# Performance work log

Measured on AMD Instinct MI355X. Metric: run time of the kernel, lower is better.

Reference implementation:

```python
import jax, jax.numpy as jnp
import numpy as np

EMBED = 1024
HEADS = 16
HEAD_DIM = EMBED // HEADS


def setup_inputs() -> dict:
    key = jax.random.key(0)
    ks = jax.random.split(key, 8)
    N, S = 4, 2048
    inp = {
        "values": jax.random.normal(ks[0], (N, S, EMBED), dtype=jnp.float32),
        "keys": jax.random.normal(ks[1], (N, S, EMBED), dtype=jnp.float32),
        "queries": jax.random.normal(ks[2], (N, S, EMBED), dtype=jnp.float32),
        # Linear weights stored as [in, out] (torch Linear applies x @ W.T; here W already transposed)
        "W_v": jax.random.normal(ks[3], (EMBED, EMBED), dtype=jnp.float32) / np.sqrt(EMBED),
        "W_k": jax.random.normal(ks[4], (EMBED, EMBED), dtype=jnp.float32) / np.sqrt(EMBED),
        "W_q": jax.random.normal(ks[5], (EMBED, EMBED), dtype=jnp.float32) / np.sqrt(EMBED),
        "W_o": jax.random.normal(ks[6], (EMBED, EMBED), dtype=jnp.float32) / np.sqrt(EMBED),
        "b_o": jax.random.normal(ks[7], (EMBED,), dtype=jnp.float32) * 0.01,
    }
    return inp


def reference(values, keys, queries, W_v, W_k, W_q, W_o, b_o):
    N, q_len, _ = queries.shape
    v = (values @ W_v).reshape(N, -1, HEADS, HEAD_DIM)   # [n, v_len, h, d]
    k = (keys @ W_k).reshape(N, -1, HEADS, HEAD_DIM)     # [n, k_len, h, d]
    q = (queries @ W_q).reshape(N, -1, HEADS, HEAD_DIM)  # [n, q_len, h, d]
    # NOTE: original scales by sqrt(embed_size), not sqrt(head_dim)
    energy = jnp.einsum('nqhd,nkhd->nhqk', q, k) / jnp.sqrt(jnp.float32(EMBED))
    attn = jax.nn.softmax(energy, axis=-1)
    out = jnp.einsum('nhqk,nkhd->nqhd', attn, v).reshape(N, q_len, EMBED)
    return out @ W_o + b_o
```

## Files before the change

kernel.cpp:

```cpp
#include <hip/hip_runtime.h>
#include <hip/hip_bf16.h>
#include <stdint.h>

typedef __attribute__((ext_vector_type(8))) short short8;
typedef __attribute__((ext_vector_type(4))) float f32x4;
typedef __attribute__((ext_vector_type(4))) unsigned short u16x4;
typedef unsigned short u16;

#define EMBED 1024
#define SEQ 2048
#define NBATCH 4
#define MROWS (NBATCH * SEQ)

__device__ __forceinline__ u16 f2bf(float f) {
  union { float f; uint32_t u; } v; v.f = f;
  uint32_t r = v.u + 0x7fffu + ((v.u >> 16) & 1u);
  return (u16)(r >> 16);
}

__device__ __forceinline__ uint32_t cvtpk(float lo, float hi) {
  uint32_t r;
  asm("v_cvt_pk_bf16_f32 %0, %1, %2" : "=v"(r) : "v"(lo), "v"(hi));
  return r;
}

__device__ __forceinline__ float vexp2(float x) {
  float r;
  asm("v_exp_f32 %0, %1" : "=v"(r) : "v"(x));
  return r;
}

__device__ __forceinline__ void gld16(const void* g, void* l) {
  __builtin_amdgcn_global_load_lds((const __attribute__((address_space(1))) void*)g,
                                   (__attribute__((address_space(3))) void*)l, 16, 0, 0);
}

__global__ __launch_bounds__(256) void prep_kernel(const float* __restrict__ W0,
                                                   const float* __restrict__ W1,
                                                   const float* __restrict__ W2,
                                                   const float* __restrict__ W3,
                                                   u16* __restrict__ T0,
                                                   u16* __restrict__ T1,
                                                   u16* __restrict__ T2,
                                                   u16* __restrict__ T3) {
  int id = blockIdx.x;
  int z = id >> 10;
  const float* W = z == 0 ? W0 : (z == 1 ? W1 : (z == 2 ? W2 : W3));
  u16* Wt = z == 0 ? T0 : (z == 1 ? T1 : (z == 2 ? T2 : T3));
  __shared__ float tile[32][33];
  int bx = (id & 31) * 32, by = ((id >> 5) & 31) * 32;
  int tx = threadIdx.x & 31, ty = threadIdx.x >> 5;
#pragma unroll
  for (int i = 0; i < 32; i += 8)
    tile[ty + i][tx] = W[(size_t)(by + ty + i) * EMBED + bx + tx];
  __syncthreads();
#pragma unroll
  for (int i = 0; i < 32; i += 8)
    Wt[(size_t)(bx + ty + i) * EMBED + by + tx] = f2bf(tile[tx][ty + i]);
}

__global__ __launch_bounds__(256) void qkv_gemm(const float* __restrict__ Aq,
                                                const float* __restrict__ Ak,
                                                const float* __restrict__ Av,
                                                const u16* __restrict__ Wqt,
                                                const u16* __restrict__ Wkt,
                                                const u16* __restrict__ Wvt,
                                                u16* __restrict__ Qb,
                                                u16* __restrict__ Kb,
                                                u16* __restrict__ Vtb,
                                                float qscale) {
  constexpr int K = 1024;
  __shared__ float lsAf[128 * 64];
  __shared__ u16 lsB[128 * 64];

  const int id = blockIdx.x;
  const int xcd = id & 7;
  const int rest = id >> 3;
  const int bx = rest & 7;
  const int p = (rest >> 3) * 8 + xcd;
  const int z = p >> 6;
  const int by = p & 63;

  const float* A = z == 0 ? Aq : (z == 1 ? Ak : Av);
  const u16* Bt  = z == 0 ? Wqt : (z == 1 ? Wkt : Wvt);
  u16* outp      = z == 0 ? Qb : (z == 1 ? Kb : Vtb);
  const float oscale = z == 0 ? qscale : 1.0f;
  const int epi = (z == 2) ? 1 : 0;

  const int t = threadIdx.x, l = t & 63, w = t >> 6;
  const int g = l >> 4, r15 = l & 15;
  const int m0 = by * 128, n0 = bx * 128;
  const int wm = (w >> 1) * 64, wn = (w & 1) * 64;
  f32x4 acc[4][4] = {};

  const int srow = t >> 3;
  const int sc16 = (t & 7) * 16;
  const u16* Bp[4];
#pragma unroll
  for (int j = 0; j < 4; ++j) {
    int row = srow + j * 32;
    int colswz = (sc16 ^ ((row & 7) << 4)) >> 1;
    Bp[j] = Bt + (size_t)(n0 + row) * K + colswz;
  }

  const int arow_b = t >> 4;
  const int au = t & 15;
  const float* Apf[8];
#pragma unroll
  for (int j = 0; j < 8; ++j) {
    int row = j * 16 + arow_b;
    int s = ((row & 7) << 1) | ((row >> 3) & 1);
    Apf[j] = A + (size_t)(m0 + row) * K + (au ^ s) * 4;
  }

  for (int k0 = 0; k0 < K; k0 += 64) {
#pragma unroll
    for (int j = 0; j < 4; ++j)
      gld16(Bp[j] + k0, lsB + j * 2048 + w * 512);
#pragma unroll
    for (int j = 0; j < 8; ++j)
      gld16(Apf[j] + k0, (char*)lsAf + j * 4096 + w * 1024);
    __syncthreads();

    short8 af[2][4], bfv[2][4];
#pragma unroll
    for (int kk = 0; kk < 2; ++kk) {
#pragma unroll
      for (int mi = 0; mi < 4; ++mi) {
        int row = wm + mi * 16 + r15;
        int s = ((row & 7) << 1) | ((row >> 3) & 1);
        int v = kk * 8 + g * 2;
        const char* base = (const char*)lsAf + row * 256;
        f32x4 a0 = *(const f32x4*)(base + ((v ^ s) * 16));
        f32x4 a1 = *(const f32x4*)(base + (((v + 1) ^ s) * 16));
        union { uint32_t u[4]; short8 sv; } pu;
        pu.u[0] = cvtpk(a0[0], a0[1]);
        pu.u[1] = cvtpk(a0[2], a0[3]);
        pu.u[2] = cvtpk(a1[0], a1[1]);
        pu.u[3] = cvtpk(a1[2], a1[3]);
        af[kk][mi] = pu.sv;
      }
#pragma unroll
      for (int ni = 0; ni < 4; ++ni) {
        int row = wn + ni * 16 + r15;
        bfv[kk][ni] = *(const short8*)((const char*)lsB + row * 128 + ((kk * 64 + g * 16) ^ ((row & 7) << 4)));
      }
    }
#pragma unroll
    for (int kk = 0; kk < 2; ++kk)
#pragma unroll
      for (int mi = 0; mi < 4; ++mi)
#pragma unroll
        for (int ni = 0; ni < 4; ++ni)
          acc[mi][ni] = __builtin_amdgcn_mfma_f32_16x16x32_bf16(af[kk][mi], bfv[kk][ni], acc[mi][ni], 0, 0, 0);
    __syncthreads();
  }

#pragma unroll
  for (int mi = 0; mi < 4; ++mi)
#pragma unroll
    for (int ni = 0; ni < 4; ++ni)
#pragma unroll
      for (int r = 0; r < 4; ++r) {
        int row = m0 + wm + mi * 16 + g * 4 + r;
        int col = n0 + wn + ni * 16 + r15;
        float v = acc[mi][ni][r];
        if (epi == 0) {
          ((u16*)outp)[(((size_t)(row >> 11) * 16 + (col >> 6)) * SEQ + (row & 2047)) * 64 + (col & 63)] = f2bf(v * oscale);
        } else {
          ((u16*)outp)[(((size_t)(row >> 11) * 16 + (col >> 6)) * 64 + (col & 63)) * SEQ + (row & 2047)] = f2bf(v);
        }
      }
}

__global__ __launch_bounds__(256) void gemm_o(const u16* __restrict__ A,
                                              const u16* __restrict__ Bt,
                                              float* __restrict__ outp,
                                              const float* __restrict__ bias) {
  constexpr int K = 1024;
  __shared__ u16 lsA[128 * 64];
  __shared__ u16 lsB[128 * 64];

  const int id = blockIdx.x;
  const int xcd = id & 7;
  const int rest = id >> 3;
  const int bx = rest & 7;
  const int by = (rest >> 3) * 8 + xcd;

  const int t = threadIdx.x, l = t & 63, w = t >> 6;
  const int g = l >> 4, r15 = l & 15;
  const int m0 = by * 128, n0 = bx * 128;
  const int wm = (w >> 1) * 64, wn = (w & 1) * 64;
  f32x4 acc[4][4] = {};
  const int srow = t >> 3;
  const int sc16 = (t & 7) * 16;

  const u16* Ap[4]; const u16* Bp[4];
#pragma unroll
  for (int j = 0; j < 4; ++j) {
    int row = srow + j * 32;
    int colswz = (sc16 ^ ((row & 7) << 4)) >> 1;
    Ap[j] = A  + (size_t)(m0 + row) * K + colswz;
    Bp[j] = Bt + (size_t)(n0 + row) * K + colswz;
  }

  for (int k0 = 0; k0 < K; k0 += 64) {
#pragma unroll
    for (int j = 0; j < 4; ++j) {
      gld16(Ap[j] + k0, lsA + j * 2048 + w * 512);
      gld16(Bp[j] + k0, lsB + j * 2048 + w * 512);
    }
    __syncthreads();
    short8 af[2][4], bfv[2][4];
#pragma unroll
    for (int kk = 0; kk < 2; ++kk) {
#pragma unroll
      for (int mi = 0; mi < 4; ++mi) {
        int row = wm + mi * 16 + r15;
        af[kk][mi] = *(const short8*)((const char*)lsA + row * 128 + ((kk * 64 + g * 16) ^ ((row & 7) << 4)));
      }
#pragma unroll
      for (int ni = 0; ni < 4; ++ni) {
        int row = wn + ni * 16 + r15;
        bfv[kk][ni] = *(const short8*)((const char*)lsB + row * 128 + ((kk * 64 + g * 16) ^ ((row & 7) << 4)));
      }
    }
#pragma unroll
    for (int kk = 0; kk < 2; ++kk)
#pragma unroll
      for (int mi = 0; mi < 4; ++mi)
#pragma unroll
        for (int ni = 0; ni < 4; ++ni)
          acc[mi][ni] = __builtin_amdgcn_mfma_f32_16x16x32_bf16(af[kk][mi], bfv[kk][ni], acc[mi][ni], 0, 0, 0);
    __syncthreads();
  }

#pragma unroll
  for (int mi = 0; mi < 4; ++mi)
#pragma unroll
    for (int ni = 0; ni < 4; ++ni)
#pragma unroll
      for (int r = 0; r < 4; ++r) {
        int row = m0 + wm + mi * 16 + g * 4 + r;
        int col = n0 + wn + ni * 16 + r15;
        outp[(size_t)row * EMBED + col] = acc[mi][ni][r] + bias[col];
      }
}

__global__ __launch_bounds__(256) void attn_kernel(const u16* __restrict__ Q,
                                                   const u16* __restrict__ Kb,
                                                   const u16* __restrict__ Vt,
                                                   u16* __restrict__ AO) {
  __shared__ u16 lsK[2][64 * 64];
  __shared__ u16 lsV[2][64 * 64];
  const int t = threadIdx.x, l = t & 63, w = t >> 6;
  const int g = l >> 4, r15 = l & 15;

  const int flat = blockIdx.x;
  const int work = (flat & 7) * 128 + (flat >> 3);
  const int bh = work >> 4;
  const int q0 = (work & 15) * 128;

  const u16* Qh = Q + (size_t)bh * SEQ * 64;
  const u16* Kh = Kb + (size_t)bh * SEQ * 64;
  const u16* Vh = Vt + (size_t)bh * 64 * SEQ;

  short8 qf[2][2];
#pragma unroll
  for (int qi = 0; qi < 2; ++qi)
#pragma unroll
    for (int dh = 0; dh < 2; ++dh)
      qf[qi][dh] = *(const short8*)&Qh[(size_t)(q0 + w * 32 + qi * 16 + r15) * 64 + dh * 32 + g * 8];

  const short8 kones = { 0x3F80, 0x3F80, 0x3F80, 0x3F80, 0x3F80, 0x3F80, 0x3F80, 0x3F80 };
  f32x4 ssum[2] = {};
  f32x4 oacc[4][2] = {};

  const int srow = t >> 3;
  const int scolb = (t & 7) * 16;

  uint4 vreg[2];

  auto STAGE_K = [&](int buf, int kv0) {
#pragma unroll
    for (int j = 0; j < 2; ++j) {
      int row = j * 32 + srow;
      int colswz = (scolb ^ ((row & 7) << 4)) >> 1;
      gld16(Kh + (size_t)(kv0 + row) * 64 + colswz, &lsK[buf][j * 2048 + w * 512]);
    }
  };
  auto VLOAD = [&](int kv0) {
#pragma unroll
    for (int j = 0; j < 2; ++j) {
      int row = j * 32 + srow;
      vreg[j] = *(const uint4*)(Vh + (size_t)row * SEQ + kv0 + (scolb >> 1));
    }
  };
  auto VSTORE = [&](int buf) {
#pragma unroll
    for (int j = 0; j < 2; ++j) {
      int row = j * 32 + srow;
      int c4 = (row & 7) << 4, c3 = ((row >> 3) & 1) << 3;
      char* base = (char*)&lsV[buf][0] + row * 128 + (scolb ^ c4);
      *(uint2*)(base + c3)       = make_uint2(vreg[j].x, vreg[j].y);
      *(uint2*)(base + (8 ^ c3)) = make_uint2(vreg[j].z, vreg[j].w);
    }
  };

  auto STEP = [&](int buf, bool pre, int a) {
    if (pre) {
      VLOAD((a + 1) * 64);
      STAGE_K(buf ^ 1, (a + 1) * 64);
    }
    const u16* Kc = lsK[buf];
    const u16* Vc = lsV[buf];

    f32x4 sacc[2][4] = {};
    __builtin_amdgcn_s_setprio(1);
#pragma unroll
    for (int c = 0; c < 4; ++c) {
      int krow = c * 16 + r15;
      int sz = (krow & 7) << 4;
#pragma unroll
      for (int dh = 0; dh < 2; ++dh) {
        short8 kf = *(const short8*)((const char*)Kc + krow * 128 + ((dh * 64 + g * 16) ^ sz));
#pragma unroll
        for (int qi = 0; qi < 2; ++qi)
          sacc[qi][c] = __builtin_amdgcn_mfma_f32_16x16x32_bf16(kf, qf[qi][dh], sacc[qi][c], 0, 0, 0);
      }
    }
    __builtin_amdgcn_s_setprio(0);

    short8 pb[2][2];
#pragma unroll
    for (int qi = 0; qi < 2; ++qi) {
#pragma unroll
      for (int c = 0; c < 4; ++c)
#pragma unroll
        for (int r = 0; r < 4; ++r)
          sacc[qi][c][r] = vexp2(sacc[qi][c][r]);
#pragma unroll
      for (int kh = 0; kh < 2; ++kh) {
        union { uint32_t u[4]; short8 s; } pu;
        pu.u[0] = cvtpk(sacc[qi][2 * kh][0],     sacc[qi][2 * kh][1]);
        pu.u[1] = cvtpk(sacc[qi][2 * kh][2],     sacc[qi][2 * kh][3]);
        pu.u[2] = cvtpk(sacc[qi][2 * kh + 1][0], sacc[qi][2 * kh + 1][1]);
        pu.u[3] = cvtpk(sacc[qi][2 * kh + 1][2], sacc[qi][2 * kh + 1][3]);
        pb[qi][kh] = pu.s;
      }
    }
#pragma unroll
    for (int qi = 0; qi < 2; ++qi)
#pragma unroll
      for (int kh = 0; kh < 2; ++kh)
        ssum[qi] = __builtin_amdgcn_mfma_f32_16x16x32_bf16(kones, pb[qi][kh], ssum[qi], 0, 0, 0);

    __builtin_amdgcn_s_setprio(1);
#pragma unroll
    for (int dc = 0; dc < 4; ++dc) {
      int vrow = dc * 16 + r15;
      int sz = ((vrow & 7) << 4) | (((vrow >> 3) & 1) << 3);
      const char* vb = (const char*)Vc + vrow * 128;
#pragma unroll
      for (int kh = 0; kh < 2; ++kh) {
        union { uint2 v[2]; short8 s; } va;
        va.v[0] = *(const uint2*)(vb + ((kh * 64 + 8 * g) ^ sz));
        va.v[1] = *(const uint2*)(vb + ((kh * 64 + 32 + 8 * g) ^ sz));
#pragma unroll
        for (int qi = 0; qi < 2; ++qi)
          oacc[dc][qi] = __builtin_amdgcn_mfma_f32_16x16x32_bf16(va.s, pb[qi][kh], oacc[dc][qi], 0, 0, 0);
      }
    }
    __builtin_amdgcn_s_setprio(0);

    if (pre) VSTORE(buf ^ 1);
    __syncthreads();
  };

  VLOAD(0);
  STAGE_K(0, 0);
  VSTORE(0);
  __syncthreads();

#pragma unroll 1
  for (int pair = 0; pair < 16; ++pair) {
    STEP(0, true, 2 * pair);
    STEP(1, pair != 15, 2 * pair + 1);
  }

  const int nb = bh >> 4, h = bh & 15;
  float inv[2] = { 1.0f / ssum[0][0], 1.0f / ssum[1][0] };
#pragma unroll
  for (int dc = 0; dc < 4; ++dc)
#pragma unroll
    for (int qi = 0; qi < 2; ++qi) {
      int q = q0 + w * 32 + qi * 16 + r15;
      int d = dc * 16 + g * 4;
      uint32_t a = cvtpk(oacc[dc][qi][0] * inv[qi], oacc[dc][qi][1] * inv[qi]);
      uint32_t b = cvtpk(oacc[dc][qi][2] * inv[qi], oacc[dc][qi][3] * inv[qi]);
      uint2* dst = (uint2*)&AO[((size_t)(nb * SEQ + q)) * EMBED + h * 64 + d];
      *dst = make_uint2(a, b);
    }
}

extern "C" void kernel_launch(void* const* d_in, const int* in_sizes, int n_in,
                              void* d_out, int out_size, void* d_ws, size_t ws_size,
                              hipStream_t stream) {
  const float* values  = (const float*)d_in[0];
  const float* keys    = (const float*)d_in[1];
  const float* queries = (const float*)d_in[2];
  const float* W_v = (const float*)d_in[3];
  const float* W_k = (const float*)d_in[4];
  const float* W_q = (const float*)d_in[5];
  const float* W_o = (const float*)d_in[6];
  const float* b_o = (const float*)d_in[7];

  const size_t XSZ = (size_t)MROWS * EMBED;
  const size_t WSZ = (size_t)EMBED * EMBED;
  u16* ws = (u16*)d_ws;
  u16* Wvt = ws;
  u16* Wkt = Wvt + WSZ;
  u16* Wqt = Wkt + WSZ;
  u16* Wot = Wqt + WSZ;
  u16* Qb  = Wot + WSZ;
  u16* Kb  = Qb + XSZ;
  u16* Vtb = Kb + XSZ;
  u16* AO  = Vtb + XSZ;

  prep_kernel<<<4096, 256, 0, stream>>>(W_v, W_k, W_q, W_o, Wvt, Wkt, Wqt, Wot);

  const float QSCALE = 0.03125f * 1.4426950408889634f;
  qkv_gemm<<<1536, 256, 0, stream>>>(queries, keys, values, Wqt, Wkt, Wvt, Qb, Kb, Vtb, QSCALE);

  attn_kernel<<<1024, 256, 0, stream>>>(Qb, Kb, Vtb, AO);

  gemm_o<<<512, 256, 0, stream>>>(AO, Wot, (float*)d_out, b_o);
}
```

Baseline: 222.4 us.

## Deepen attention K/V prefetch to two tiles ahead with triple-buffered K

Restructures the attention loop so K tiles are triple-buffered in LDS and V tiles are double-buffered in registers, prefetching two KV tiles ahead instead of one. Uses explicit vmcnt/lgkmcnt waits and a raw s_barrier instead of __syncthreads, so the async loads can stay in flight across the barrier. The goal is to hide global-load latency behind MFMA work. In exchange it uses more LDS and registers, which may lower occupancy, and the hand-counted waitcnt values must match the number of loads issued or the results will be wrong.

```diff
diff --git a/kernel.cpp b/kernel.cpp
--- a/kernel.cpp
+++ b/kernel.cpp
@@ -251,7 +251,7 @@
                                                    const u16* __restrict__ Kb,
                                                    const u16* __restrict__ Vt,
                                                    u16* __restrict__ AO) {
-  __shared__ u16 lsK[2][64 * 64];
+  __shared__ u16 lsK[3][64 * 64];
   __shared__ u16 lsV[2][64 * 64];
   const int t = threadIdx.x, l = t & 63, w = t >> 6;
   const int g = l >> 4, r15 = l & 15;
@@ -279,7 +279,7 @@
   const int srow = t >> 3;
   const int scolb = (t & 7) * 16;
 
-  uint4 vreg[2];
+  uint4 vreg[2][2];
 
   auto STAGE_K = [&](int buf, int kv0) {
 #pragma unroll
@@ -289,32 +289,25 @@
       gld16(Kh + (size_t)(kv0 + row) * 64 + colswz, &lsK[buf][j * 2048 + w * 512]);
     }
   };
-  auto VLOAD = [&](int kv0) {
+  auto VLOAD = [&](int par, int kv0) {
 #pragma unroll
     for (int j = 0; j < 2; ++j) {
       int row = j * 32 + srow;
-      vreg[j] = *(const uint4*)(Vh + (size_t)row * SEQ + kv0 + (scolb >> 1));
+      vreg[par][j] = *(const uint4*)(Vh + (size_t)row * SEQ + kv0 + (scolb >> 1));
     }
   };
-  auto VSTORE = [&](int buf) {
+  auto VSTORE = [&](int buf, int par) {
 #pragma unroll
     for (int j = 0; j < 2; ++j) {
       int row = j * 32 + srow;
       int c4 = (row & 7) << 4, c3 = ((row >> 3) & 1) << 3;
       char* base = (char*)&lsV[buf][0] + row * 128 + (scolb ^ c4);
-      *(uint2*)(base + c3)       = make_uint2(vreg[j].x, vreg[j].y);
-      *(uint2*)(base + (8 ^ c3)) = make_uint2(vreg[j].z, vreg[j].w);
+      *(uint2*)(base + c3)       = make_uint2(vreg[par][j].x, vreg[par][j].y);
+      *(uint2*)(base + (8 ^ c3)) = make_uint2(vreg[par][j].z, vreg[par][j].w);
     }
   };
 
-  auto STEP = [&](int buf, bool pre, int a) {
-    if (pre) {
-      VLOAD((a + 1) * 64);
-      STAGE_K(buf ^ 1, (a + 1) * 64);
-    }
-    const u16* Kc = lsK[buf];
-    const u16* Vc = lsV[buf];
-
+  auto COMPUTE = [&](const u16* Kc, const u16* Vc) {
     f32x4 sacc[2][4] = {};
     __builtin_amdgcn_s_setprio(1);
 #pragma unroll
@@ -372,21 +365,44 @@
       }
     }
     __builtin_amdgcn_s_setprio(0);
-
-    if (pre) VSTORE(buf ^ 1);
-    __syncthreads();
   };
 
-  VLOAD(0);
-  STAGE_K(0, 0);
-  VSTORE(0);
-  __syncthreads();
+  auto STEP = [&](int tt, int kb, int vb, bool stv, bool ld) {
+    if (stv) VSTORE((tt + 1) & 1, (tt + 1) & 1);
+    if (ld) {
+      VLOAD(tt & 1, (tt + 2) * 64);
+      STAGE_K((tt + 2) % 3, (tt + 2) * 64);
+    }
+    COMPUTE(lsK[kb], lsV[vb]);
+    if (tt < 31) {
+      if (ld) asm volatile("s_waitcnt vmcnt(4)" ::: "memory");
+      else    asm volatile("s_waitcnt vmcnt(0)" ::: "memory");
+      asm volatile("s_waitcnt lgkmcnt(0)" ::: "memory");
+      __builtin_amdgcn_s_barrier();
+      __builtin_amdgcn_sched_barrier(0);
+    }
+  };
+
+  VLOAD(0, 0);        STAGE_K(0, 0);
+  VLOAD(1, 64);       STAGE_K(1, 64);
+  VSTORE(0, 0);
+  asm volatile("s_waitcnt vmcnt(4)" ::: "memory");
+  asm volatile("s_waitcnt lgkmcnt(0)" ::: "memory");
+  __builtin_amdgcn_s_barrier();
+  __builtin_amdgcn_sched_barrier(0);
 
 #pragma unroll 1
-  for (int pair = 0; pair < 16; ++pair) {
-    STEP(0, true, 2 * pair);
-    STEP(1, pair != 15, 2 * pair + 1);
-  }
+  for (int it = 0; it < 5; ++it) {
+    int base = it * 6;
+    STEP(base + 0, 0, 0, true, true);
+    STEP(base + 1, 1, 1, true, true);
+    STEP(base + 2, 2, 0, true, true);
+    STEP(base + 3, 0, 1, true, true);
+    STEP(base + 4, 1, 0, true, true);
+    STEP(base + 5, 2, 1, true, true);
+  }
+  STEP(30, 0, 0, true, false);
+  STEP(31, 1, 1, false, false);
 
   const int nb = bh >> 4, h = bh & 15;
   float inv[2] = { 1.0f / ssum[0][0], 1.0f / ssum[1][0] };
```

Result: faster. 209.8 us (-5.7%).

## Read K fragments directly from global memory and deepen V register prefetch

Applied to the files above, without the earlier changes.

The attention kernel stops staging K tiles through shared memory. Each lane now loads its K MFMA fragments straight from global memory, relying on L1/L2 caching. V tiles are still staged through LDS, but with two register buffers so loads run two steps ahead, and the per-step sync placement is reworked. This removes LDS traffic and the async copies for K, at the cost of more global/L1 load latency inside the QK^T loop and more registers.

```diff
diff --git a/kernel.cpp b/kernel.cpp
--- a/kernel.cpp
+++ b/kernel.cpp
@@ -4,7 +4,6 @@
 
 typedef __attribute__((ext_vector_type(8))) short short8;
 typedef __attribute__((ext_vector_type(4))) float f32x4;
-typedef __attribute__((ext_vector_type(4))) unsigned short u16x4;
 typedef unsigned short u16;
 
 #define EMBED 1024
@@ -251,7 +250,6 @@
                                                    const u16* __restrict__ Kb,
                                                    const u16* __restrict__ Vt,
                                                    u16* __restrict__ AO) {
-  __shared__ u16 lsK[2][64 * 64];
   __shared__ u16 lsV[2][64 * 64];
   const int t = threadIdx.x, l = t & 63, w = t >> 6;
   const int g = l >> 4, r15 = l & 15;
@@ -279,51 +277,38 @@
   const int srow = t >> 3;
   const int scolb = (t & 7) * 16;
 
-  uint4 vreg[2];
-
-  auto STAGE_K = [&](int buf, int kv0) {
+  uint4 vreg[2][2];
+
+  const u16* Kr = Kh + (size_t)r15 * 64 + g * 8;
+
+  auto VLOAD = [&](int par, int kv0) {
 #pragma unroll
     for (int j = 0; j < 2; ++j) {
       int row = j * 32 + srow;
-      int colswz = (scolb ^ ((row & 7) << 4)) >> 1;
-      gld16(Kh + (size_t)(kv0 + row) * 64 + colswz, &lsK[buf][j * 2048 + w * 512]);
+      vreg[par][j] = *(const uint4*)(Vh + (size_t)row * SEQ + kv0 + (scolb >> 1));
     }
   };
-  auto VLOAD = [&](int kv0) {
-#pragma unroll
-    for (int j = 0; j < 2; ++j) {
-      int row = j * 32 + srow;
-      vreg[j] = *(const uint4*)(Vh + (size_t)row * SEQ + kv0 + (scolb >> 1));
-    }
-  };
-  auto VSTORE = [&](int buf) {
+  auto VSTORE = [&](int buf, int par) {
 #pragma unroll
     for (int j = 0; j < 2; ++j) {
       int row = j * 32 + srow;
       int c4 = (row & 7) << 4, c3 = ((row >> 3) & 1) << 3;
       char* base = (char*)&lsV[buf][0] + row * 128 + (scolb ^ c4);
-      *(uint2*)(base + c3)       = make_uint2(vreg[j].x, vreg[j].y);
-      *(uint2*)(base + (8 ^ c3)) = make_uint2(vreg[j].z, vreg[j].w);
+      *(uint2*)(base + c3)       = make_uint2(vreg[par][j].x, vreg[par][j].y);
+      *(uint2*)(base + (8 ^ c3)) = make_uint2(vreg[par][j].z, vreg[par][j].w);
     }
   };
 
-  auto STEP = [&](int buf, bool pre, int a) {
-    if (pre) {
-      VLOAD((a + 1) * 64);
-      STAGE_K(buf ^ 1, (a + 1) * 64);
-    }
-    const u16* Kc = lsK[buf];
-    const u16* Vc = lsV[buf];
+  auto COMPUTE = [&](int kv, const u16* Vc) {
+    const u16* Kt = Kr + (size_t)kv * 4096;
 
     f32x4 sacc[2][4] = {};
     __builtin_amdgcn_s_setprio(1);
 #pragma unroll
     for (int c = 0; c < 4; ++c) {
-      int krow = c * 16 + r15;
-      int sz = (krow & 7) << 4;
 #pragma unroll
       for (int dh = 0; dh < 2; ++dh) {
-        short8 kf = *(const short8*)((const char*)Kc + krow * 128 + ((dh * 64 + g * 16) ^ sz));
+        short8 kf = *(const short8*)(Kt + (size_t)c * 1024 + dh * 32);
 #pragma unroll
         for (int qi = 0; qi < 2; ++qi)
           sacc[qi][c] = __builtin_amdgcn_mfma_f32_16x16x32_bf16(kf, qf[qi][dh], sacc[qi][c], 0, 0, 0);
@@ -372,20 +357,19 @@
       }
     }
     __builtin_amdgcn_s_setprio(0);
-
-    if (pre) VSTORE(buf ^ 1);
-    __syncthreads();
   };
 
-  VLOAD(0);
-  STAGE_K(0, 0);
-  VSTORE(0);
+  VLOAD(0, 0);
+  VSTORE(0, 0);
+  VLOAD(1, 64);
   __syncthreads();
 
-#pragma unroll 1
-  for (int pair = 0; pair < 16; ++pair) {
-    STEP(0, true, 2 * pair);
-    STEP(1, pair != 15, 2 * pair + 1);
+#pragma unroll 2
+  for (int kv = 0; kv < 32; ++kv) {
+    if (kv < 31) VSTORE((kv + 1) & 1, (kv + 1) & 1);
+    if (kv < 30) VLOAD(kv & 1, (kv + 2) * 64);
+    COMPUTE(kv, lsV[kv & 1]);
+    if (kv < 31) __syncthreads();
   }
 
   const int nb = bh >> 4, h = bh & 15;
```

Measured after the change: 291.1 us. +30.9%, slower.
